# Kernel tuning notes

Measured on AMD Instinct MI355X. Metric: run time of the kernel, lower is better.

The kernel has to match this reference:

```python
import jax, jax.numpy as jnp
import numpy as np

B, C, N, K = 4, 192, 8192, 16
C_OUT = 192


def _gather_nodes(xs, idx):
    # xs: [B, C, N], idx: [B, N, K] -> [B, C, N, K]
    return jax.vmap(lambda xb, ib: xb[:, ib])(xs, idx)


def setup_inputs() -> dict:
    key = jax.random.key(0)
    k1, k2, k3 = jax.random.split(key, 3)
    x = jax.random.normal(k1, (B, C, N, 1), dtype=jnp.float32)
    x_0 = jnp.zeros((B, C, N, 1), dtype=jnp.float32)  # unused by forward, kept for interface
    edge_index = jax.random.randint(k2, (2, B, N, K), 0, N, dtype=jnp.int32)
    # 1x1 Conv2d(2C -> C_OUT) weight flattened to [C_OUT, 2C]
    W = jax.random.normal(k3, (C_OUT, 2 * C), dtype=jnp.float32) / np.sqrt(2 * C)
    b = jnp.zeros((C_OUT,), dtype=jnp.float32)
    return {"x": x, "x_0": x_0, "edge_index": edge_index, "W": W, "b": b}


def reference(x, x_0, edge_index, W, b):
    xs = x[..., 0]                       # [B, C, N]
    x_i = _gather_nodes(xs, edge_index[1])   # centers  [B, C, N, K]
    x_j = _gather_nodes(xs, edge_index[0])   # neighbors [B, C, N, K]
    rel = jnp.max(x_j - x_i, axis=-1)        # max-relative [B, C, N]
    y = jnp.concatenate([xs, rel], axis=1)   # [B, 2C, N]
    out = jnp.einsum('oc,bcn->bon', W, y) + b[None, :, None]  # 1x1 conv
    out = jax.nn.relu(out)
    return out[..., None]                # [B, C_OUT, N, 1]
```

## Files before the change

### kernel.cpp

```cpp
#include <hip/hip_runtime.h>
#include <hip/hip_fp16.h>

#define B_    4
#define C_    192
#define N_    8192
#define K_    16
#define O_    192
#define TWOC_ 384

typedef __attribute__((ext_vector_type(8))) _Float16 half8;
typedef __attribute__((ext_vector_type(4))) _Float16 half4v;
typedef __attribute__((ext_vector_type(4))) float floatx4;

#define NINF ((_Float16)(-65504.0f))

__global__ __launch_bounds__(256) void k_convert_w(const float* __restrict__ W,
                                                   unsigned short* __restrict__ Wb) {
    int i = blockIdx.x * 256 + threadIdx.x;
    if (i < O_ * TWOC_) {
        union { _Float16 h; unsigned short s; } v;
        v.h = (_Float16)W[i];
        Wb[i] = v.s;
    }
}

__global__ __launch_bounds__(256) void k_transpose(const float* __restrict__ x,
                                                   unsigned short* __restrict__ xt) {
    __shared__ float tile[32][33];
    int bid  = blockIdx.x;
    int xcd  = bid & 7;
    int b    = xcd >> 1;
    int half = xcd & 1;
    int slot = bid >> 3;
    int ct   = slot >> 7;
    int nt   = half * 128 + (slot & 127);
    int c0 = ct * 32, n0 = nt * 32;
    int tid = threadIdx.x;

    int cc  = tid >> 3;
    int nn4 = (tid & 7) * 4;
    const float* xp = x + ((size_t)b * C_ + c0 + cc) * N_ + n0 + nn4;
    float4 v = *(const float4*)xp;
    tile[nn4 + 0][cc] = v.x;
    tile[nn4 + 1][cc] = v.y;
    tile[nn4 + 2][cc] = v.z;
    tile[nn4 + 3][cc] = v.w;
    __syncthreads();

#pragma unroll
    for (int i = 0; i < 2; i++) {
        int id  = i * 256 + tid;
        int row = id >> 4;
        int ch2 = id & 15;
        union { _Float16 h[2]; unsigned int u; } p;
        p.h[0] = (_Float16)tile[row][ch2 * 2];
        p.h[1] = (_Float16)tile[row][ch2 * 2 + 1];
        *(unsigned int*)(xt + ((size_t)b * N_ + n0 + row) * C_ + c0 + ch2 * 2) = p.u;
    }
}

__global__ __launch_bounds__(256, 4) void k_fused(const unsigned short* __restrict__ xt,
                                                  const int* __restrict__ eidx,
                                                  const unsigned short* __restrict__ Wb,
                                                  const float* __restrict__ bias,
                                                  float* __restrict__ out) {
    __shared__ __align__(16) unsigned short rtile[32][192];
    __shared__ int sidx[32][33];

    int bid  = blockIdx.x;
    int xcd  = bid & 7;
    int b    = xcd >> 1;
    int slot = bid >> 3;
    int n0   = ((xcd & 1) * 128 + slot) * 32;

    int tid  = threadIdx.x;
    int wave = tid >> 6;
    int lane = tid & 63;
    int m16  = lane & 15;
    int quad = lane >> 4;

    const int* e0 = eidx + ((size_t)b * N_ + n0) * K_;
    const int* e1 = e0 + (size_t)B_ * N_ * K_;
#pragma unroll
    for (int i = 0; i < 2; i++) {
        int id = i * 256 + tid;
        int node = id >> 4, k = id & 15;
        sidx[node][k]      = e0[id];
        sidx[node][16 + k] = e1[id];
    }

    floatx4 acc[3][2];
#pragma unroll
    for (int i = 0; i < 3; i++)
#pragma unroll
        for (int j = 0; j < 2; j++) acc[i][j] = (floatx4){0.f, 0.f, 0.f, 0.f};

    const unsigned short* wbase = Wb + (size_t)(wave * 48 + m16) * TWOC_ + quad * 8;
    const unsigned short* ybase = xt + ((size_t)b * N_ + n0 + m16) * C_ + quad * 8;

#pragma unroll 2
    for (int kt = 0; kt < 6; kt++) {
        half8 wf[3], yf[2];
#pragma unroll
        for (int i = 0; i < 3; i++)
            wf[i] = *(const half8*)(wbase + (size_t)(i * 16) * TWOC_ + kt * 32);
#pragma unroll
        for (int j = 0; j < 2; j++)
            yf[j] = *(const half8*)(ybase + (size_t)(j * 16) * C_ + kt * 32);
#pragma unroll
        for (int i = 0; i < 3; i++)
#pragma unroll
            for (int j = 0; j < 2; j++)
                acc[i][j] = __builtin_amdgcn_mfma_f32_16x16x32_f16(wf[i], yf[j], acc[i][j], 0, 0, 0);
    }

    __syncthreads();

    {
        const unsigned short* xbase = xt + (size_t)b * N_ * C_;
        int g = quad, l4 = m16;
#pragma unroll
        for (int bb = 0; bb < 2; bb++) {
            int node = wave * 8 + bb * 4 + g;
            half8  m0 = {NINF, NINF, NINF, NINF, NINF, NINF, NINF, NINF};
            half4v m1 = {NINF, NINF, NINF, NINF};
#pragma unroll
            for (int k = 0; k < K_; k++) {
                int jn  = sidx[node][k];
                int in_ = sidx[node][16 + k];
                const unsigned short* pj = xbase + (size_t)jn * C_;
                const unsigned short* pi = xbase + (size_t)in_ * C_;
                half8  a0 = *(const half8*)(pj + l4 * 8);
                half8  b0 = *(const half8*)(pi + l4 * 8);
                half4v a1 = *(const half4v*)(pj + 128 + l4 * 4);
                half4v b1 = *(const half4v*)(pi + 128 + l4 * 4);
                m0 = __builtin_elementwise_max(m0, a0 - b0);
                m1 = __builtin_elementwise_max(m1, a1 - b1);
            }
            char* rb = (char*)rtile + node * 384;
            unsigned int sw = (unsigned)(node & 7) << 4;
            *(half8*)(rb + ((unsigned)(l4 * 16) ^ sw))        = m0;
            *(half4v*)(rb + ((unsigned)(256 + l4 * 8) ^ sw))  = m1;
        }
    }
    __syncthreads();

#pragma unroll 2
    for (int kt = 0; kt < 6; kt++) {
        half8 wf[3], yf[2];
#pragma unroll
        for (int i = 0; i < 3; i++)
            wf[i] = *(const half8*)(wbase + (size_t)(i * 16) * TWOC_ + (C_ + kt * 32));
#pragma unroll
        for (int j = 0; j < 2; j++) {
            int r = j * 16 + m16;
            unsigned int off = (unsigned)(kt * 64 + quad * 16) ^ ((unsigned)(r & 7) << 4);
            yf[j] = *(const half8*)((char*)rtile + (size_t)r * 384 + off);
        }
#pragma unroll
        for (int i = 0; i < 3; i++)
#pragma unroll
            for (int j = 0; j < 2; j++)
                acc[i][j] = __builtin_amdgcn_mfma_f32_16x16x32_f16(wf[i], yf[j], acc[i][j], 0, 0, 0);
    }

#pragma unroll
    for (int i = 0; i < 3; i++) {
#pragma unroll
        for (int r = 0; r < 4; r++) {
            int o = wave * 48 + i * 16 + quad * 4 + r;
            float bv = bias[o];
#pragma unroll
            for (int j = 0; j < 2; j++) {
                int n = n0 + j * 16 + m16;
                out[((size_t)b * O_ + o) * N_ + n] = fmaxf(acc[i][j][r] + bv, 0.f);
            }
        }
    }
}

extern "C" void kernel_launch(void* const* d_in, const int* in_sizes, int n_in,
                              void* d_out, int out_size, void* d_ws, size_t ws_size,
                              hipStream_t stream) {
    const float* x    = (const float*)d_in[0];
    const int*   eidx = (const int*)d_in[2];
    const float* W    = (const float*)d_in[3];
    const float* bias = (const float*)d_in[4];
    float*       out  = (float*)d_out;

    unsigned short* Wb = (unsigned short*)d_ws;
    unsigned short* xt = (unsigned short*)((char*)d_ws + 147456);

    k_convert_w<<<dim3((O_ * TWOC_ + 255) / 256), dim3(256), 0, stream>>>(W, Wb);
    k_transpose<<<dim3(6144), dim3(256), 0, stream>>>(x, xt);
    k_fused<<<dim3(1024), dim3(256), 0, stream>>>(xt, eidx, Wb, bias, out);
}
```

Before: 139.3 us.

## Merge prep kernels, redistribute gather across k with shuffles, use nontemporal memory ops

Merges the weight conversion and transpose into one launch, which removes a kernel launch. The gather-max stage is rebuilt so that each wave handles one node at a time, with the 16 neighbors split across the four quads and combined by xor shuffles, and it now runs before the first GEMM half. Index loading is vectorized, and nontemporal loads and stores are used for the streaming data. In exchange, the kernel adds shuffle and cross-lane reduction overhead, and only one quad in four performs the LDS writes.

```diff
diff --git a/kernel.cpp b/kernel.cpp
--- a/kernel.cpp
+++ b/kernel.cpp
@@ -7,27 +7,55 @@
 #define K_    16
 #define O_    192
 #define TWOC_ 384
+#define BN_   (B_ * N_)
 
 typedef __attribute__((ext_vector_type(8))) _Float16 half8;
 typedef __attribute__((ext_vector_type(4))) _Float16 half4v;
 typedef __attribute__((ext_vector_type(4))) float floatx4;
-
-#define NINF ((_Float16)(-65504.0f))
-
-__global__ __launch_bounds__(256) void k_convert_w(const float* __restrict__ W,
-                                                   unsigned short* __restrict__ Wb) {
-    int i = blockIdx.x * 256 + threadIdx.x;
-    if (i < O_ * TWOC_) {
-        union { _Float16 h; unsigned short s; } v;
-        v.h = (_Float16)W[i];
-        Wb[i] = v.s;
-    }
-}
-
-__global__ __launch_bounds__(256) void k_transpose(const float* __restrict__ x,
-                                                   unsigned short* __restrict__ xt) {
+typedef __attribute__((ext_vector_type(4))) float fvec4;
+typedef __attribute__((ext_vector_type(4))) int   ivec4;
+typedef __attribute__((ext_vector_type(4))) unsigned int uvec4;
+
+static __device__ __forceinline__ half8 shflx8(half8 v, int m) {
+    union { half8 h; int i[4]; } u;
+    u.h = v;
+#pragma unroll
+    for (int q = 0; q < 4; q++) u.i[q] = __shfl_xor(u.i[q], m, 64);
+    return u.h;
+}
+static __device__ __forceinline__ half4v shflx4(half4v v, int m) {
+    union { half4v h; int i[2]; } u;
+    u.h = v;
+#pragma unroll
+    for (int q = 0; q < 2; q++) u.i[q] = __shfl_xor(u.i[q], m, 64);
+    return u.h;
+}
+
+__global__ __launch_bounds__(256) void k_prep(const float* __restrict__ x,
+                                              const float* __restrict__ W,
+                                              unsigned short* __restrict__ xt,
+                                              unsigned short* __restrict__ Wb) {
+    int bid = blockIdx.x;
+    int tid = threadIdx.x;
+
+    if (bid >= 6144) {
+        int base = ((bid - 6144) * 256 + tid) * 16;
+        union { unsigned short u[16]; uvec4 v[2]; } o;
+#pragma unroll
+        for (int q = 0; q < 16; q += 4) {
+            fvec4 f = __builtin_nontemporal_load((const fvec4*)(W + base + q));
+            union { _Float16 h; unsigned short s; } c;
+            c.h = (_Float16)f.x; o.u[q + 0] = c.s;
+            c.h = (_Float16)f.y; o.u[q + 1] = c.s;
+            c.h = (_Float16)f.z; o.u[q + 2] = c.s;
+            c.h = (_Float16)f.w; o.u[q + 3] = c.s;
+        }
+        *(uvec4*)(Wb + base)     = o.v[0];
+        *(uvec4*)(Wb + base + 8) = o.v[1];
+        return;
+    }
+
     __shared__ float tile[32][33];
-    int bid  = blockIdx.x;
     int xcd  = bid & 7;
     int b    = xcd >> 1;
     int half = xcd & 1;
@@ -35,12 +63,11 @@
     int ct   = slot >> 7;
     int nt   = half * 128 + (slot & 127);
     int c0 = ct * 32, n0 = nt * 32;
-    int tid = threadIdx.x;
 
     int cc  = tid >> 3;
     int nn4 = (tid & 7) * 4;
     const float* xp = x + ((size_t)b * C_ + c0 + cc) * N_ + n0 + nn4;
-    float4 v = *(const float4*)xp;
+    fvec4 v = __builtin_nontemporal_load((const fvec4*)xp);
     tile[nn4 + 0][cc] = v.x;
     tile[nn4 + 1][cc] = v.y;
     tile[nn4 + 2][cc] = v.z;
@@ -64,8 +91,9 @@
                                                   const unsigned short* __restrict__ Wb,
                                                   const float* __restrict__ bias,
                                                   float* __restrict__ out) {
-    __shared__ __align__(16) unsigned short rtile[32][192];
-    __shared__ int sidx[32][33];
+    __shared__ __align__(16) unsigned short rtile[32 * C_];
+    __shared__ __align__(16) int sidx[32][36];
+    char* rb0 = (char*)rtile;
 
     int bid  = blockIdx.x;
     int xcd  = bid & 7;
@@ -79,24 +107,69 @@
     int m16  = lane & 15;
     int quad = lane >> 4;
 
-    const int* e0 = eidx + ((size_t)b * N_ + n0) * K_;
-    const int* e1 = e0 + (size_t)B_ * N_ * K_;
-#pragma unroll
-    for (int i = 0; i < 2; i++) {
-        int id = i * 256 + tid;
-        int node = id >> 4, k = id & 15;
-        sidx[node][k]      = e0[id];
-        sidx[node][16 + k] = e1[id];
-    }
-
-    floatx4 acc[3][2];
-#pragma unroll
-    for (int i = 0; i < 3; i++)
-#pragma unroll
-        for (int j = 0; j < 2; j++) acc[i][j] = (floatx4){0.f, 0.f, 0.f, 0.f};
+    {
+        const int* e0 = eidx + ((size_t)b * N_ + n0) * K_;
+        const int* e1 = e0 + (size_t)BN_ * K_;
+        int side = tid >> 7;
+        int id   = tid & 127;
+        const int* src = side ? e1 : e0;
+        ivec4 v = __builtin_nontemporal_load((const ivec4*)src + id);
+        int node = id >> 2, kq = (id & 3) * 4;
+        *(ivec4*)&sidx[node][side * 16 + kq] = v;
+    }
+    __syncthreads();
+
+    {
+        int kg = quad, part = m16;
+        const unsigned short* xb = xt + (size_t)b * N_ * C_;
+#pragma unroll 2
+        for (int nn = 0; nn < 8; nn++) {
+            int node = wave * 8 + nn;
+            ivec4 j4 = *(const ivec4*)&sidx[node][kg * 4];
+            ivec4 i4 = *(const ivec4*)&sidx[node][16 + kg * 4];
+            half8  m0;
+            half4v m1;
+#pragma unroll
+            for (int it = 0; it < 4; it++) {
+                int jn  = j4[it];
+                int in_ = i4[it];
+                const unsigned short* pj = xb + (size_t)jn * C_;
+                const unsigned short* pi = xb + (size_t)in_ * C_;
+                half8  a0 = *(const half8*)(pj + part * 8);
+                half4v a1 = *(const half4v*)(pj + 128 + part * 4);
+                half8  b0 = *(const half8*)(pi + part * 8);
+                half4v b1 = *(const half4v*)(pi + 128 + part * 4);
+                half8  d0 = a0 - b0;
+                half4v d1 = a1 - b1;
+                if (it == 0) { m0 = d0; m1 = d1; }
+                else {
+                    m0 = __builtin_elementwise_max(m0, d0);
+                    m1 = __builtin_elementwise_max(m1, d1);
+                }
+            }
+            m0 = __builtin_elementwise_max(m0, shflx8(m0, 16));
+            m1 = __builtin_elementwise_max(m1, shflx4(m1, 16));
+            m0 = __builtin_elementwise_max(m0, shflx8(m0, 32));
+            m1 = __builtin_elementwise_max(m1, shflx4(m1, 32));
+
+            if (kg == 0) {
+                char* rb = rb0 + node * 384;
+                unsigned int sw = (unsigned)(node & 7) << 4;
+                *(half8*)(rb + ((unsigned)(part * 16) ^ sw))       = m0;
+                *(half4v*)(rb + ((unsigned)(256 + part * 8) ^ sw)) = m1;
+            }
+        }
+    }
+    __syncthreads();
 
     const unsigned short* wbase = Wb + (size_t)(wave * 48 + m16) * TWOC_ + quad * 8;
     const unsigned short* ybase = xt + ((size_t)b * N_ + n0 + m16) * C_ + quad * 8;
+
+    floatx4 acc[3][2];
+#pragma unroll
+    for (int i = 0; i < 3; i++)
+#pragma unroll
+        for (int j = 0; j < 2; j++) acc[i][j] = (floatx4){0.f, 0.f, 0.f, 0.f};
 
 #pragma unroll 2
     for (int kt = 0; kt < 6; kt++) {
@@ -114,37 +187,6 @@
                 acc[i][j] = __builtin_amdgcn_mfma_f32_16x16x32_f16(wf[i], yf[j], acc[i][j], 0, 0, 0);
     }
 
-    __syncthreads();
-
-    {
-        const unsigned short* xbase = xt + (size_t)b * N_ * C_;
-        int g = quad, l4 = m16;
-#pragma unroll
-        for (int bb = 0; bb < 2; bb++) {
-            int node = wave * 8 + bb * 4 + g;
-            half8  m0 = {NINF, NINF, NINF, NINF, NINF, NINF, NINF, NINF};
-            half4v m1 = {NINF, NINF, NINF, NINF};
-#pragma unroll
-            for (int k = 0; k < K_; k++) {
-                int jn  = sidx[node][k];
-                int in_ = sidx[node][16 + k];
-                const unsigned short* pj = xbase + (size_t)jn * C_;
-                const unsigned short* pi = xbase + (size_t)in_ * C_;
-                half8  a0 = *(const half8*)(pj + l4 * 8);
-                half8  b0 = *(const half8*)(pi + l4 * 8);
-                half4v a1 = *(const half4v*)(pj + 128 + l4 * 4);
-                half4v b1 = *(const half4v*)(pi + 128 + l4 * 4);
-                m0 = __builtin_elementwise_max(m0, a0 - b0);
-                m1 = __builtin_elementwise_max(m1, a1 - b1);
-            }
-            char* rb = (char*)rtile + node * 384;
-            unsigned int sw = (unsigned)(node & 7) << 4;
-            *(half8*)(rb + ((unsigned)(l4 * 16) ^ sw))        = m0;
-            *(half4v*)(rb + ((unsigned)(256 + l4 * 8) ^ sw))  = m1;
-        }
-    }
-    __syncthreads();
-
 #pragma unroll 2
     for (int kt = 0; kt < 6; kt++) {
         half8 wf[3], yf[2];
@@ -154,8 +196,8 @@
 #pragma unroll
         for (int j = 0; j < 2; j++) {
             int r = j * 16 + m16;
-            unsigned int off = (unsigned)(kt * 64 + quad * 16) ^ ((unsigned)(r & 7) << 4);
-            yf[j] = *(const half8*)((char*)rtile + (size_t)r * 384 + off);
+            yf[j] = *(const half8*)(rb0 + (size_t)r * 384 +
+                                    (((unsigned)(kt * 64 + quad * 16)) ^ ((unsigned)(r & 7) << 4)));
         }
 #pragma unroll
         for (int i = 0; i < 3; i++)
@@ -173,7 +215,8 @@
 #pragma unroll
             for (int j = 0; j < 2; j++) {
                 int n = n0 + j * 16 + m16;
-                out[((size_t)b * O_ + o) * N_ + n] = fmaxf(acc[i][j][r] + bv, 0.f);
+                __builtin_nontemporal_store(fmaxf(acc[i][j][r] + bv, 0.f),
+                                            &out[((size_t)b * O_ + o) * N_ + n]);
             }
         }
     }
@@ -191,7 +234,6 @@
     unsigned short* Wb = (unsigned short*)d_ws;
     unsigned short* xt = (unsigned short*)((char*)d_ws + 147456);
 
-    k_convert_w<<<dim3((O_ * TWOC_ + 255) / 256), dim3(256), 0, stream>>>(W, Wb);
-    k_transpose<<<dim3(6144), dim3(256), 0, stream>>>(x, xt);
+    k_prep<<<dim3(6162), dim3(256), 0, stream>>>(x, W, xt, Wb);
     k_fused<<<dim3(1024), dim3(256), 0, stream>>>(xt, eidx, Wb, bias, out);
 }
```

After: 138.5 us. About the same (-0.6%).
